# Kernel tuning notes

Hardware: AMD Instinct MI355X
Metric: run time of the kernel (lower is better)

## Reference

```python
import jax, jax.numpy as jnp
import numpy as np

EPSILON = 1e-8
MATCH_THRESHOLD = 0.5
MEANINGFUL_RADIUS = 0.05


def setup_inputs() -> dict:
    key = jax.random.key(0)
    ks = jax.random.split(key, 8)
    B, T, H, D, N = 4, 4096, 2048, 256, 8192
    K = H // 4
    s = lambda k, shape, fan_in: jax.random.normal(k, shape, jnp.float32) * (fan_in ** -0.5)
    return {
        "hidden": jax.random.normal(ks[0], (B, T, H), jnp.float32),
        "beliefs": jax.random.normal(ks[1], (N, D), jnp.float32),
        "active_mask": jax.random.bernoulli(ks[2], 0.9, (N,)),
        "W_obs": s(ks[3], (D, H), H),
        "W_g1": s(ks[4], (K, H), H),
        "b_g1": jnp.zeros((K,), jnp.float32),
        "W_g2": s(ks[5], (1, K), K),
        "b_g2": jnp.full((1,), -2.0, jnp.float32),  # nn.init.constant_(bias, -2.0)
        "W_p1": s(ks[6], (K, H), H),
        "b_p1": jnp.zeros((K,), jnp.float32),
        "W_p2": s(ks[7], (1, K), K),
        "b_p2": jnp.zeros((1,), jnp.float32),
    }


def reference(hidden, beliefs, active_mask, W_obs, W_g1, b_g1, W_g2, b_g2, W_p1, b_p1, W_p2, b_p2):
    # --- projections over [B, T, H] ---
    obs = jnp.einsum('bth,dh->btd', hidden, W_obs)                       # [B,T,D]
    g_h = jax.nn.relu(jnp.einsum('bth,kh->btk', hidden, W_g1) + b_g1)
    gate = jax.nn.sigmoid(jnp.einsum('btk,ok->bto', g_h, W_g2) + b_g2)   # [B,T,1]
    p_h = jax.nn.relu(jnp.einsum('bth,kh->btk', hidden, W_p1) + b_p1)
    prec = jax.nn.softplus(jnp.einsum('btk,ok->bto', p_h, W_p2) + b_p2)  # [B,T,1]

    obs_mean = obs.mean(axis=0)            # [T,D]
    prec_mean = (gate * prec).mean(axis=0)  # [T,1]

    # F.normalize(x, dim=-1, eps) == x / max(||x||, eps)
    obs_angles = obs_mean / jnp.maximum(
        jnp.linalg.norm(obs_mean, axis=-1, keepdims=True), EPSILON)
    obs_beliefs = obs_angles * prec_mean    # [T,D], radius = gated precision

    # --- match against active belief slots (fully vectorized, no per-token loop) ---
    obs_r = jnp.linalg.norm(obs_beliefs, axis=-1)                       # [T]
    obs_ang = obs_beliefs / jnp.maximum(obs_r, EPSILON)[:, None]
    bel_r = jnp.maximum(jnp.linalg.norm(beliefs, axis=-1), EPSILON)     # [N]
    bel_ang = beliefs / bel_r[:, None]

    sims = obs_ang @ bel_ang.T              # [T,N] cosine similarities
    neg = jnp.finfo(sims.dtype).min
    masked = jnp.where(active_mask[None, :], sims, neg)
    any_active = jnp.any(active_mask)
    best_sims = jnp.where(any_active, masked.max(axis=-1), 0.0)         # [T]
    best_idx = jnp.where(any_active, jnp.argmax(masked, axis=-1), -1)   # [T]

    meaningful = obs_r > MEANINGFUL_RADIUS
    matched = meaningful & (best_sims > MATCH_THRESHOLD)
    matched_slot = jnp.where(matched, best_idx, -1)                     # -1 == new slot
    match_sim = jnp.where(matched, best_sims, 0.0)

    # vectorized stand-in for list[WriteCandidate]:
    # belief vectors, per-token match similarity, matched slot id, validity mask
    return obs_beliefs, match_sim, matched_slot, meaningful
```

## Files before the change

### kernel.cpp

```cpp
#include <hip/hip_runtime.h>

constexpr int B = 4, T = 4096, H = 2048, D = 256, KK = 512, N = 8192;
constexpr int BT = B * T;
constexpr int NALL = 1280;
constexpr int CAP = 1024;
constexpr int MCAP = 256;

typedef short bf16x8 __attribute__((ext_vector_type(8)));
typedef float f32x4  __attribute__((ext_vector_type(4)));

__device__ __forceinline__ unsigned short f2bf(float f) {
    unsigned u = __float_as_uint(f);
    return (unsigned short)((u + 0x7fffu + ((u >> 16) & 1u)) >> 16);
}
__device__ __forceinline__ float bf2f(unsigned short h) {
    return __uint_as_float((unsigned)h << 16);
}
__device__ __forceinline__ void async16(const void* g, void* l) {
    __builtin_amdgcn_global_load_lds(
        (const __attribute__((address_space(1))) unsigned int*)g,
        (__attribute__((address_space(3))) unsigned int*)l, 16, 0, 0);
}
__device__ __forceinline__ unsigned long long enc_sim(float s, int idx) {
    unsigned bits = __float_as_uint(s);
    unsigned e32 = (bits & 0x80000000u) ? ~bits : (bits | 0x80000000u);
    return ((unsigned long long)e32 << 32) | (unsigned)(~(unsigned)idx);
}
__device__ __forceinline__ unsigned enc_f32(float s) {
    unsigned b = __float_as_uint(s);
    return (b & 0x80000000u) ? ~b : (b | 0x80000000u);
}
__device__ __forceinline__ float dec_f32(unsigned e) {
    return __uint_as_float((e & 0x80000000u) ? (e & 0x7FFFFFFFu) : ~e);
}

constexpr size_t WS_HB   = 0;
constexpr size_t WS_WB   = WS_HB   + (size_t)BT * H * 2;
constexpr size_t WS_BELB = WS_WB   + (size_t)NALL * H * 2;
constexpr size_t WS_OAB  = WS_BELB + (size_t)N * D * 2;
constexpr size_t WS_OBS  = WS_OAB  + (size_t)T * D * 2;
constexpr size_t WS_B1C  = WS_OBS  + (size_t)T * D * 4;
constexpr size_t WS_W2C  = WS_B1C  + 4096;
constexpr size_t WS_FAC  = WS_W2C  + 4096;
constexpr size_t WS_OBSR = WS_FAC  + 16384;
constexpr size_t WS_FLAG = WS_OBSR + 16384;
constexpr size_t WS_ACTV = WS_FLAG + (size_t)CAP * 4;
constexpr size_t WS_META = WS_ACTV + (size_t)N * 4;
constexpr size_t WS_YG   = WS_META + 256;
constexpr size_t WS_YP   = WS_YG   + (size_t)BT * 4;
constexpr size_t WS_ENC  = WS_YP   + (size_t)BT * 4;
constexpr size_t WS_CNT  = WS_ENC  + (size_t)T * 4;
constexpr size_t WS_MCNT = WS_CNT  + 256;
constexpr size_t WS_MLST = WS_MCNT + 256;
constexpr size_t WS_ZEND = WS_MLST + (size_t)MCAP * 4;
constexpr size_t WS_NEEDF = WS_ZEND;
constexpr size_t WS_ZEROSZ = WS_ZEND - WS_YG;

constexpr int    WTC    = 1280;
constexpr size_t F_WT   = 0;
constexpr size_t F_BEL  = F_WT   + (size_t)H * WTC * 4;
constexpr size_t F_OBS  = F_BEL  + (size_t)N * D * 4;
constexpr size_t F_YG   = F_OBS  + (size_t)T * D * 4;
constexpr size_t F_YP   = F_YG   + (size_t)BT * 4;
constexpr size_t F_OBSR = F_YP   + (size_t)BT * 4;
constexpr size_t F_ENC  = F_OBSR + (size_t)T * 4;
constexpr size_t F_ACT  = F_ENC  + (size_t)T * 8;
constexpr size_t F_META = F_ACT  + (size_t)N * 4;
constexpr size_t F_NEED = F_META + 256;

__global__ void mask_kernel(const unsigned char* raw, int* active, int* meta) {
    __shared__ int s_f32bad, s_nz_nonaligned;
    if (threadIdx.x == 0) { s_f32bad = 0; s_nz_nonaligned = 0; }
    __syncthreads();
    const float* rf = (const float*)raw;
    const int*   ri = (const int*)raw;
    for (int i = threadIdx.x; i < N; i += blockDim.x) {
        unsigned char b = raw[i];
        if ((i & 3) && b) atomicOr(&s_nz_nonaligned, 1);
    }
    for (int e = threadIdx.x; e < N / 4; e += blockDim.x) {
        float f = rf[e]; if (!(f == 0.0f || f == 1.0f)) atomicOr(&s_f32bad, 1);
    }
    __syncthreads();
    int layout;
    if (!s_f32bad)            layout = 2;
    else if (s_nz_nonaligned) layout = 1;
    else                      layout = 0;
    for (int n = threadIdx.x; n < N; n += blockDim.x) {
        int a;
        if (layout == 2)      a = (rf[n] != 0.0f);
        else if (layout == 1) a = (raw[n] != 0);
        else                  a = (ri[n] != 0);
        active[n] = a;
    }
    if (threadIdx.x == 0) meta[0] = layout;
}

__global__ void conv_hidden(const float* hidden, unsigned short* hb) {
    int e = blockIdx.x * 256 + threadIdx.x;
    int row = e >> 8, c8 = (e & 255) * 8;
    const float* src = hidden + (size_t)row * H + c8;
    float4 v0 = *(const float4*)src;
    float4 v1 = *(const float4*)(src + 4);
    uint4 o;
    o.x = f2bf(v0.x) | ((unsigned)f2bf(v0.y) << 16);
    o.y = f2bf(v0.z) | ((unsigned)f2bf(v0.w) << 16);
    o.z = f2bf(v1.x) | ((unsigned)f2bf(v1.y) << 16);
    o.w = f2bf(v1.z) | ((unsigned)f2bf(v1.w) << 16);
    *(uint4*)(hb + (size_t)row * H + c8) = o;
}

__global__ void conv_wb(const float* Wg1, const float* Wp1, const float* Wobs,
                        unsigned short* wb) {
    int e = blockIdx.x * 256 + threadIdx.x;
    int row = e >> 8, c8 = (e & 255) * 8;
    const float* src = (row < 512) ? &Wg1[(size_t)row * H]
                     : (row < 1024) ? &Wp1[(size_t)(row - 512) * H]
                                    : &Wobs[(size_t)(row - 1024) * H];
    float4 v0 = *(const float4*)(src + c8);
    float4 v1 = *(const float4*)(src + c8 + 4);
    uint4 o;
    o.x = f2bf(v0.x) | ((unsigned)f2bf(v0.y) << 16);
    o.y = f2bf(v0.z) | ((unsigned)f2bf(v0.w) << 16);
    o.z = f2bf(v1.x) | ((unsigned)f2bf(v1.y) << 16);
    o.w = f2bf(v1.z) | ((unsigned)f2bf(v1.w) << 16);
    *(uint4*)(wb + (size_t)row * H + c8) = o;
}

__global__ void conv_vec(const float* b_g1, const float* b_p1, const float* W_g2,
                         const float* W_p2, float* b1c, float* w2c) {
    int c = threadIdx.x;
    if (c < 512) { b1c[c] = b_g1[c];       w2c[c] = W_g2[c]; }
    else         { b1c[c] = b_p1[c - 512]; w2c[c] = W_p2[c - 512]; }
}

__global__ void belprep_bf(const float* beliefs, unsigned short* belb) {
    int wave = (blockIdx.x * blockDim.x + threadIdx.x) >> 6;
    int lane = threadIdx.x & 63;
    if (wave >= N) return;
    float4 v = ((const float4*)(beliefs + (size_t)wave * D))[lane];
    float ss = v.x * v.x + v.y * v.y + v.z * v.z + v.w * v.w;
    for (int m = 1; m < 64; m <<= 1) ss += __shfl_xor(ss, m, 64);
    float inv = 1.0f / fmaxf(sqrtf(ss), 1e-8f);
    uint2 o;
    o.x = f2bf(v.x * inv) | ((unsigned)f2bf(v.y * inv) << 16);
    o.y = f2bf(v.z * inv) | ((unsigned)f2bf(v.w * inv) << 16);
    *(uint2*)(belb + (size_t)wave * D + lane * 4) = o;
}

__global__ __launch_bounds__(256) void gemm_mlp_mfma(const unsigned short* Ab, const unsigned short* Bb,
                                                     const float* b1c, const float* w2c,
                                                     float* yg, float* yp) {
    __shared__ unsigned short As[128 * 32];
    __shared__ unsigned short Bs[128 * 32];
    __shared__ float b1s[128], w2s[128];
    int tid = threadIdx.x;
    int mb = blockIdx.x, nb = blockIdx.y;
    int m0 = mb * 128, n0 = nb * 128;
    if (tid < 128) { b1s[tid] = b1c[n0 + tid]; w2s[tid] = w2c[n0 + tid]; }
    int wave = tid >> 6, lane = tid & 63;
    int wr = wave >> 1, wc = wave & 1;
    int quad = lane >> 4, mrow = lane & 15;
    f32x4 acc[4][4] = {};
    const unsigned short* gA = Ab + (size_t)(m0 + (tid >> 2)) * H + (tid & 3) * 8;
    const unsigned short* gB = Bb + (size_t)(n0 + (tid >> 2)) * H + (tid & 3) * 8;
    char* lA = (char*)As + wave * 1024;
    char* lB = (char*)Bs + wave * 1024;
    for (int k0 = 0; k0 < H; k0 += 32) {
        async16(gA + k0, lA);
        async16(gA + (size_t)64 * H + k0, lA + 4096);
        async16(gB + k0, lB);
        async16(gB + (size_t)64 * H + k0, lB + 4096);
        __syncthreads();
        bf16x8 a[4], b[4];
        for (int i = 0; i < 4; i++) a[i] = *(const bf16x8*)&As[(wr * 64 + i * 16 + mrow) * 32 + quad * 8];
        for (int j = 0; j < 4; j++) b[j] = *(const bf16x8*)&Bs[(wc * 64 + j * 16 + mrow) * 32 + quad * 8];
        for (int i = 0; i < 4; i++)
            for (int j = 0; j < 4; j++)
                acc[i][j] = __builtin_amdgcn_mfma_f32_16x16x32_bf16(a[i], b[j], acc[i][j], 0, 0, 0);
        __syncthreads();
    }
    float* y = (nb < 4) ? yg : yp;
    for (int i = 0; i < 4; i++) {
        int row_g = m0 + wr * 64 + i * 16 + quad * 4;
        for (int r = 0; r < 4; r++) {
            float s = 0.0f;
            for (int j = 0; j < 4; j++) {
                int cl = wc * 64 + j * 16 + mrow;
                float z = fmaxf(acc[i][j][r] + b1s[cl], 0.0f);
                s += z * w2s[cl];
            }
            s += __shfl_xor(s, 1); s += __shfl_xor(s, 2);
            s += __shfl_xor(s, 4); s += __shfl_xor(s, 8);
            if (mrow == 0) atomicAdd(&y[row_g + r], s);
        }
    }
}

__global__ __launch_bounds__(512) void gemm_obs_sum(const unsigned short* hb, const unsigned short* wb,
                                                    float* obs_buf) {
    __shared__ unsigned short As[128 * 32];
    __shared__ unsigned short Bs[256 * 32];
    int tid = threadIdx.x;
    int t0 = blockIdx.x * 128;
    int wave = tid >> 6, lane = tid & 63;
    int wr = wave >> 2, wc = wave & 3;
    int quad = lane >> 4, mrow = lane & 15;
    f32x4 acc[4][4] = {};
    int arow = tid >> 2, seg8 = (tid & 3) * 8;
    const unsigned short* hA = hb + (size_t)(t0 + arow) * H + seg8;
    const unsigned short* gB = wb + (size_t)(1024 + (tid >> 2)) * H + (tid & 3) * 8;
    char* lB = (char*)Bs + wave * 1024;
    for (int k0 = 0; k0 < H; k0 += 32) {
        async16(gB + k0, lB);
        async16(gB + (size_t)128 * H + k0, lB + 8192);
        {
            uint4 v0 = *(const uint4*)(hA + k0);
            uint4 v1 = *(const uint4*)(hA + (size_t)T * H + k0);
            uint4 v2 = *(const uint4*)(hA + (size_t)2 * T * H + k0);
            uint4 v3 = *(const uint4*)(hA + (size_t)3 * T * H + k0);
            const unsigned* p0 = (const unsigned*)&v0;
            const unsigned* p1 = (const unsigned*)&v1;
            const unsigned* p2 = (const unsigned*)&v2;
            const unsigned* p3 = (const unsigned*)&v3;
            uint4 o; unsigned* po = (unsigned*)&o;
            for (int q = 0; q < 4; q++) {
                float lo = 0.25f * (bf2f((unsigned short)(p0[q] & 0xFFFF)) + bf2f((unsigned short)(p1[q] & 0xFFFF))
                                  + bf2f((unsigned short)(p2[q] & 0xFFFF)) + bf2f((unsigned short)(p3[q] & 0xFFFF)));
                float hi = 0.25f * (bf2f((unsigned short)(p0[q] >> 16)) + bf2f((unsigned short)(p1[q] >> 16))
                                  + bf2f((unsigned short)(p2[q] >> 16)) + bf2f((unsigned short)(p3[q] >> 16)));
                po[q] = f2bf(lo) | ((unsigned)f2bf(hi) << 16);
            }
            *(uint4*)&As[arow * 32 + seg8] = o;
        }
        __syncthreads();
        bf16x8 a[4], b[4];
        for (int i = 0; i < 4; i++) a[i] = *(const bf16x8*)&As[(wr * 64 + i * 16 + mrow) * 32 + quad * 8];
        for (int j = 0; j < 4; j++) b[j] = *(const bf16x8*)&Bs[(wc * 64 + j * 16 + mrow) * 32 + quad * 8];
        for (int i = 0; i < 4; i++)
            for (int j = 0; j < 4; j++)
                acc[i][j] = __builtin_amdgcn_mfma_f32_16x16x32_bf16(a[i], b[j], acc[i][j], 0, 0, 0);
        __syncthreads();
    }
    for (int i = 0; i < 4; i++)
        for (int r = 0; r < 4; r++) {
            int row_g = t0 + wr * 64 + i * 16 + quad * 4 + r;
            for (int j = 0; j < 4; j++) {
                int col = wc * 64 + j * 16 + mrow;
                obs_buf[(size_t)row_g * D + col] = acc[i][j][r];
            }
        }
}

__global__ void finalize_fast(const float* yg, const float* yp, const float* obs_buf,
                              const float* b_g2, const float* b_p2,
                              float* out0, float* out3, float* obs_r_ws, float* fac,
                              unsigned short* oab, int* flaglist, int* flagcnt,
                              float* yg_mut, float* yp_mut) {
    int t = blockIdx.x * 4 + (threadIdx.x >> 6);
    int lane = threadIdx.x & 63;
    if (t >= T) return;
    float bg2 = b_g2[0], bp2 = b_p2[0];
    float pm = 0.0f;
    for (int b = 0; b < B; ++b) {
        float g = yg[b * T + t] + bg2;
        float p = yp[b * T + t] + bp2;
        float gate = 1.0f / (1.0f + expf(-g));
        float prec = (p > 20.0f) ? p : log1pf(expf(p));
        pm += gate * prec;
    }
    pm *= 0.25f;
    float4 v = ((const float4*)(obs_buf + (size_t)t * D))[lane];
    float ss = v.x * v.x + v.y * v.y + v.z * v.z + v.w * v.w;
    for (int m = 1; m < 64; m <<= 1) ss += __shfl_xor(ss, m, 64);
    float norm = sqrtf(ss);
    float na = fmaxf(norm, 1e-8f);
    float f = norm / na;
    float inv = 1.0f / na;
    float ax = v.x * inv, ay = v.y * inv, az = v.z * inv, aw = v.w * inv;
    float4 ob; ob.x = ax * pm; ob.y = ay * pm; ob.z = az * pm; ob.w = aw * pm;
    ((float4*)(out0 + (size_t)t * D))[lane] = ob;
    uint2 oa;
    oa.x = f2bf(ax) | ((unsigned)f2bf(ay) << 16);
    oa.y = f2bf(az) | ((unsigned)f2bf(aw) << 16);
    *(uint2*)(oab + (size_t)t * D + lane * 4) = oa;
    if (lane == 0) {
        float obs_r = pm * f;
        obs_r_ws[t] = obs_r;
        fac[t] = f;
        out3[t] = (obs_r > 0.05f) ? 1.0f : 0.0f;
        if (fabsf(obs_r - 0.05f) < 5.0e-4f) {
            int idx = atomicAdd(flagcnt, 1);
            if (idx < CAP) {
                flaglist[idx] = t;
                for (int b = 0; b < B; ++b) { yg_mut[b * T + t] = 0.0f; yp_mut[b * T + t] = 0.0f; }
            }
        }
    }
}

__global__ __launch_bounds__(256) void refine_mfma(const float* hidden,
        const float* W_g1, const float* W_p1, const float* b1c, const float* w2c,
        const int* flaglist, const int* flagcnt, float* yg, float* yp) {
    int nrows = min(*flagcnt, CAP) * 4;
    int m0 = blockIdx.x * 64;
    if (m0 >= nrows) return;
    int nb = blockIdx.y;
    int n0 = nb * 128;
    __shared__ unsigned short Ahi[64 * 32], Alo[64 * 32];
    __shared__ unsigned short Bhi[128 * 32], Blo[128 * 32];
    __shared__ int rowg_s[64];
    __shared__ float b1s[128], w2s[128];
    int tid = threadIdx.x;
    if (tid < 64) {
        int fr = m0 + tid;
        int rg = -1;
        if (fr < nrows) { int tok = flaglist[fr >> 2]; rg = (fr & 3) * T + tok; }
        rowg_s[tid] = rg;
    } else if (tid >= 128) {
        int c = tid - 128;
        b1s[c] = b1c[n0 + c]; w2s[c] = w2c[n0 + c];
    }
    __syncthreads();
    const float* Wbase = (n0 < 512) ? W_g1 : W_p1;
    int wofs = n0 & 511;
    int arow = tid >> 2, kseg = (tid & 3) * 8;
    int argr = rowg_s[arow]; if (argr < 0) argr = 0;
    const float* aptr = hidden + (size_t)argr * H + kseg;
    const float* bptr0 = Wbase + (size_t)(wofs + arow) * H + kseg;
    const float* bptr1 = Wbase + (size_t)(wofs + arow + 64) * H + kseg;
    int wave = tid >> 6, lane = tid & 63;
    int quad = lane >> 4, mrow = lane & 15;
    f32x4 acc[4][2] = {};
    for (int k0 = 0; k0 < H; k0 += 32) {
        float xs[8];
        {
            float4 v0 = *(const float4*)(aptr + k0);
            float4 v1 = *(const float4*)(aptr + k0 + 4);
            xs[0]=v0.x; xs[1]=v0.y; xs[2]=v0.z; xs[3]=v0.w;
            xs[4]=v1.x; xs[5]=v1.y; xs[6]=v1.z; xs[7]=v1.w;
            unsigned short hi[8], lo[8];
            for (int q = 0; q < 8; q++) {
                hi[q] = f2bf(xs[q]);
                lo[q] = f2bf(xs[q] - bf2f(hi[q]));
            }
            uint4 ph, pl;
            ph.x = hi[0]|((unsigned)hi[1]<<16); ph.y = hi[2]|((unsigned)hi[3]<<16);
            ph.z = hi[4]|((unsigned)hi[5]<<16); ph.w = hi[6]|((unsigned)hi[7]<<16);
            pl.x = lo[0]|((unsigned)lo[1]<<16); pl.y = lo[2]|((unsigned)lo[3]<<16);
            pl.z = lo[4]|((unsigned)lo[5]<<16); pl.w = lo[6]|((unsigned)lo[7]<<16);
            *(uint4*)&Ahi[arow * 32 + kseg] = ph;
            *(uint4*)&Alo[arow * 32 + kseg] = pl;
        }
        for (int half = 0; half < 2; half++) {
            const float* bp = half ? bptr1 : bptr0;
            float4 v0 = *(const float4*)(bp + k0);
            float4 v1 = *(const float4*)(bp + k0 + 4);
            xs[0]=v0.x; xs[1]=v0.y; xs[2]=v0.z; xs[3]=v0.w;
            xs[4]=v1.x; xs[5]=v1.y; xs[6]=v1.z; xs[7]=v1.w;
            unsigned short hi[8], lo[8];
            for (int q = 0; q < 8; q++) {
                hi[q] = f2bf(xs[q]);
                lo[q] = f2bf(xs[q] - bf2f(hi[q]));
            }
            uint4 ph, pl;
            ph.x = hi[0]|((unsigned)hi[1]<<16); ph.y = hi[2]|((unsigned)hi[3]<<16);
            ph.z = hi[4]|((unsigned)hi[5]<<16); ph.w = hi[6]|((unsigned)hi[7]<<16);
            pl.x = lo[0]|((unsigned)lo[1]<<16); pl.y = lo[2]|((unsigned)lo[3]<<16);
            pl.z = lo[4]|((unsigned)lo[5]<<16); pl.w = lo[6]|((unsigned)lo[7]<<16);
            *(uint4*)&Bhi[(arow + half * 64) * 32 + kseg] = ph;
            *(uint4*)&Blo[(arow + half * 64) * 32 + kseg] = pl;
        }
        __syncthreads();
        bf16x8 ah[4], al[4], bh[2], bl[2];
        for (int i = 0; i < 4; i++) {
            ah[i] = *(const bf16x8*)&Ahi[(i * 16 + mrow) * 32 + quad * 8];
            al[i] = *(const bf16x8*)&Alo[(i * 16 + mrow) * 32 + quad * 8];
        }
        for (int j = 0; j < 2; j++) {
            bh[j] = *(const bf16x8*)&Bhi[(wave * 32 + j * 16 + mrow) * 32 + quad * 8];
            bl[j] = *(const bf16x8*)&Blo[(wave * 32 + j * 16 + mrow) * 32 + quad * 8];
        }
        for (int i = 0; i < 4; i++)
            for (int j = 0; j < 2; j++) {
                acc[i][j] = __builtin_amdgcn_mfma_f32_16x16x32_bf16(al[i], bh[j], acc[i][j], 0, 0, 0);
                acc[i][j] = __builtin_amdgcn_mfma_f32_16x16x32_bf16(ah[i], bl[j], acc[i][j], 0, 0, 0);
                acc[i][j] = __builtin_amdgcn_mfma_f32_16x16x32_bf16(ah[i], bh[j], acc[i][j], 0, 0, 0);
            }
        __syncthreads();
    }
    float* y = (nb < 4) ? yg : yp;
    for (int i = 0; i < 4; i++)
        for (int r = 0; r < 4; r++) {
            int row_l = i * 16 + quad * 4 + r;
            float s = 0.0f;
            for (int j = 0; j < 2; j++) {
                int cl = wave * 32 + j * 16 + mrow;
                float z = fmaxf(acc[i][j][r] + b1s[cl], 0.0f);
                s += z * w2s[cl];
            }
            s += __shfl_xor(s, 1); s += __shfl_xor(s, 2);
            s += __shfl_xor(s, 4); s += __shfl_xor(s, 8);
            if (mrow == 0) {
                int rg = rowg_s[row_l];
                if (rg >= 0) atomicAdd(&y[rg], s);
            }
        }
}

__global__ void refine_pm(const float* yg, const float* yp, const float* b_g2, const float* b_p2,
                          const int* flagcnt, const int* flaglist, const float* fac,
                          float* obs_r_ws, float* out3) {
    int nflag = min(*flagcnt, CAP);
    int idx = blockIdx.x * 64 + threadIdx.x;
    if (idx >= nflag) return;
    int t = flaglist[idx];
    float bg2 = b_g2[0], bp2 = b_p2[0];
    float pm = 0.0f;
    for (int b = 0; b < B; ++b) {
        float g = yg[b * T + t] + bg2;
        float p = yp[b * T + t] + bp2;
        float gate = 1.0f / (1.0f + expf(-g));
        float prec = (p > 20.0f) ? p : log1pf(expf(p));
        pm += gate * prec;
    }
    pm *= 0.25f;
    float obs_r = pm * fac[t];
    obs_r_ws[t] = obs_r;
    out3[t] = (obs_r > 0.05f) ? 1.0f : 0.0f;
}

__global__ __launch_bounds__(256) void sims_mfma(const unsigned short* oab, const unsigned short* belb,
                                                 const int* active, unsigned* encg) {
    __shared__ unsigned short As[128 * 32];
    __shared__ unsigned short Bs[128 * 32];
    __shared__ int acts[128];
    __shared__ unsigned lmax32[128];
    int tid = threadIdx.x;
    int mb = blockIdx.x, nb = blockIdx.y;
    int m0 = mb * 128, n0 = nb * 128;
    if (tid < 128) { acts[tid] = active[n0 + tid]; lmax32[tid] = 0u; }
    int wave = tid >> 6, lane = tid & 63;
    int wr = wave >> 1, wc = wave & 1;
    int quad = lane >> 4, mrow = lane & 15;
    f32x4 acc[4][4] = {};
    const unsigned short* gA = oab + (size_t)(m0 + (tid >> 2)) * D + (tid & 3) * 8;
    const unsigned short* gB = belb + (size_t)(n0 + (tid >> 2)) * D + (tid & 3) * 8;
    char* lA = (char*)As + wave * 1024;
    char* lB = (char*)Bs + wave * 1024;
    for (int k0 = 0; k0 < D; k0 += 32) {
        async16(gA + k0, lA);
        async16(gA + (size_t)64 * D + k0, lA + 4096);
        async16(gB + k0, lB);
        async16(gB + (size_t)64 * D + k0, lB + 4096);
        __syncthreads();
        bf16x8 a[4], b[4];
        for (int i = 0; i < 4; i++) a[i] = *(const bf16x8*)&As[(wr * 64 + i * 16 + mrow) * 32 + quad * 8];
        for (int j = 0; j < 4; j++) b[j] = *(const bf16x8*)&Bs[(wc * 64 + j * 16 + mrow) * 32 + quad * 8];
        for (int i = 0; i < 4; i++)
            for (int j = 0; j < 4; j++)
                acc[i][j] = __builtin_amdgcn_mfma_f32_16x16x32_bf16(a[i], b[j], acc[i][j], 0, 0, 0);
        __syncthreads();
    }
    for (int i = 0; i < 4; i++)
        for (int r = 0; r < 4; r++) {
            int row_l = wr * 64 + i * 16 + quad * 4 + r;
            float m = -3.4e38f;
            for (int j = 0; j < 4; j++) {
                int cl = wc * 64 + j * 16 + mrow;
                if (acts[cl]) m = fmaxf(m, acc[i][j][r]);
            }
            m = fmaxf(m, __shfl_xor(m, 1)); m = fmaxf(m, __shfl_xor(m, 2));
            m = fmaxf(m, __shfl_xor(m, 4)); m = fmaxf(m, __shfl_xor(m, 8));
            if (mrow == 0 && m > -3.3e38f) atomicMax(&lmax32[row_l], enc_f32(m));
        }
    __syncthreads();
    if (tid < 128 && lmax32[tid]) atomicMax(&encg[m0 + tid], lmax32[tid]);
}

__global__ void outw_kernel(const unsigned* encg, const float* obs_r_ws,
                            float* out1, float* out2, int* mcnt, int* mlist) {
    int t = blockIdx.x * 256 + threadIdx.x;
    if (t >= T) return;
    unsigned ev = encg[t];
    float best = (ev == 0u) ? -3.4e38f : dec_f32(ev);
    bool meaningful = obs_r_ws[t] > 0.05f;
    bool matched = meaningful && (best > 0.5f);
    out1[t] = matched ? best : 0.0f;
    out2[t] = -1.0f;
    if (matched) {
        int slot = atomicAdd(mcnt, 1);
        if (slot < MCAP) mlist[slot] = t;
    }
}

__global__ void argmax_kernel(const unsigned short* oab, const unsigned short* belb,
                              const int* active, const int* mcnt, const int* mlist,
                              float* out1, float* out2) {
    int nm = min(*mcnt, MCAP);
    int j = blockIdx.x;
    if (j >= nm) return;
    int t = mlist[j];
    __shared__ float q[256];
    __shared__ unsigned long long red[256];
    if (threadIdx.x < 128) {
        unsigned v = ((const unsigned*)(oab + (size_t)t * D))[threadIdx.x];
        q[threadIdx.x * 2]     = bf2f((unsigned short)(v & 0xFFFF));
        q[threadIdx.x * 2 + 1] = bf2f((unsigned short)(v >> 16));
    }
    __syncthreads();
    float best = -3.4e38f; int bi = -1;
    for (int k = 0; k < N / 256; k++) {
        int n = threadIdx.x + k * 256;
        if (!active[n]) continue;
        const uint4* br = (const uint4*)(belb + (size_t)n * D);
        float s = 0.0f;
        for (int c = 0; c < 32; c++) {
            uint4 v = br[c];
            const unsigned* pv = (const unsigned*)&v;
            for (int w = 0; w < 4; w++) {
                s += q[c * 8 + w * 2]     * bf2f((unsigned short)(pv[w] & 0xFFFF));
                s += q[c * 8 + w * 2 + 1] * bf2f((unsigned short)(pv[w] >> 16));
            }
        }
        if (s > best) { best = s; bi = n; }
    }
    red[threadIdx.x] = (bi >= 0) ? enc_sim(best, bi) : 0ULL;
    __syncthreads();
    for (int st = 128; st > 0; st >>= 1) {
        if (threadIdx.x < st) red[threadIdx.x] = max(red[threadIdx.x], red[threadIdx.x + st]);
        __syncthreads();
    }
    if (threadIdx.x == 0) {
        unsigned long long ev = red[0];
        if (ev) {
            unsigned e32 = (unsigned)(ev >> 32);
            out1[t] = __uint_as_float((e32 & 0x80000000u) ? (e32 & 0x7FFFFFFFu) : ~e32);
            out2[t] = (float)(int)~((unsigned)(ev & 0xFFFFFFFFu));
        }
    }
}

__global__ void f_mask_kernel(const unsigned char* raw, int* active, int* meta) {
    __shared__ int s_f32bad, s_nz_nonaligned;
    if (threadIdx.x == 0) { s_f32bad = 0; s_nz_nonaligned = 0; }
    __syncthreads();
    const float* rf = (const float*)raw;
    const int*   ri = (const int*)raw;
    for (int i = threadIdx.x; i < N; i += blockDim.x) {
        unsigned char b = raw[i];
        if ((i & 3) && b) atomicOr(&s_nz_nonaligned, 1);
    }
    for (int e = threadIdx.x; e < N / 4; e += blockDim.x) {
        float f = rf[e]; if (!(f == 0.0f || f == 1.0f)) atomicOr(&s_f32bad, 1);
    }
    __syncthreads();
    int layout = (!s_f32bad) ? 2 : (s_nz_nonaligned ? 1 : 0);
    for (int n = threadIdx.x; n < N; n += blockDim.x) {
        int a;
        if (layout == 2)      a = (rf[n] != 0.0f);
        else if (layout == 1) a = (raw[n] != 0);
        else                  a = (ri[n] != 0);
        active[n] = a;
    }
    if (threadIdx.x == 0) meta[0] = layout;
}

__global__ void wt_kernel(const float* Wg1, const float* Wp1, const float* Wobs, float* WT) {
    __shared__ float tile[32][33];
    int hb = blockIdx.x * 32, cb = blockIdx.y * 32;
    int x = threadIdx.x & 31, y = threadIdx.x >> 5;
    for (int i = 0; i < 32; i += 8) {
        int c = cb + y + i;
        const float* src = (c < 512) ? &Wg1[(size_t)c * H]
                         : (c < 1024) ? &Wp1[(size_t)(c - 512) * H]
                                      : &Wobs[(size_t)(c - 1024) * H];
        tile[y + i][x] = src[hb + x];
    }
    __syncthreads();
    for (int i = 0; i < 32; i += 8)
        WT[(size_t)(hb + y + i) * WTC + cb + x] = tile[x][y + i];
}

__global__ void belprep_kernel(const float* beliefs, float* bel_ang) {
    int wave = (blockIdx.x * blockDim.x + threadIdx.x) >> 6;
    int lane = threadIdx.x & 63;
    if (wave >= N) return;
    float4 v = ((const float4*)(beliefs + (size_t)wave * D))[lane];
    float ss = v.x * v.x + v.y * v.y + v.z * v.z + v.w * v.w;
    for (int m = 1; m < 64; m <<= 1) ss += __shfl_xor(ss, m, 64);
    float inv = 1.0f / fmaxf(sqrtf(ss), 1e-8f);
    float4 o; o.x = v.x * inv; o.y = v.y * inv; o.z = v.z * inv; o.w = v.w * inv;
    ((float4*)(bel_ang + (size_t)wave * D))[lane] = o;
}

__global__ __launch_bounds__(256) void gemm_obs_kernel(const float* hidden, const float* WT,
                                                       float* obs_mean) {
    __shared__ float As[32][33];
    __shared__ float Ws[32][260];
    int t0 = blockIdx.x * 32;
    int tx = threadIdx.x & 63, ty = threadIdx.x >> 6;
    float acc[8][4] = {};
    for (int h0 = 0; h0 < H; h0 += 32) {
        for (int q = 0; q < 4; ++q) {
            int e = threadIdx.x + q * 256;
            int r = e >> 5, kk = e & 31;
            float s = 0.0f;
            for (int b = 0; b < B; ++b) s += hidden[((size_t)b * T + t0 + r) * H + h0 + kk];
            As[kk][r] = s;
        }
        for (int q = 0; q < 8; ++q) {
            int e4 = threadIdx.x + q * 256;
            int kk = e4 >> 6, c4 = (e4 & 63) * 4;
            *(float4*)&Ws[kk][c4] = *(const float4*)&WT[(size_t)(h0 + kk) * WTC + 1024 + c4];
        }
        __syncthreads();
        for (int kk = 0; kk < 32; ++kk) {
            float a[8], w[4];
            for (int i = 0; i < 8; i++) a[i] = As[kk][ty * 8 + i];
            for (int j = 0; j < 4; j++) w[j] = Ws[kk][tx + 64 * j];
            for (int i = 0; i < 8; i++)
                for (int j = 0; j < 4; j++) acc[i][j] += a[i] * w[j];
        }
        __syncthreads();
    }
    for (int i = 0; i < 8; i++)
        for (int j = 0; j < 4; j++)
            obs_mean[(size_t)(t0 + ty * 8 + i) * D + tx + 64 * j] = acc[i][j] * 0.25f;
}

__global__ __launch_bounds__(512, 4) void gemm_mlp_kernel(
        const float* hidden, const float* WT,
        const float* b1g, const float* b1p, const float* w2g, const float* w2p,
        const float* b2g, const float* b2p, float* yg, float* yp) {
    __shared__ float As[16][65];
    __shared__ float Ws[16][516];
    int R = blockIdx.x * 64;
    int path = blockIdx.y;
    int cbase = path * 512;
    int tx = threadIdx.x & 63, ty = threadIdx.x >> 6;
    float acc[8][8] = {};
    for (int h0 = 0; h0 < H; h0 += 16) {
        {   int r = threadIdx.x >> 3, k2 = (threadIdx.x & 7) * 2;
            float2 v = *(const float2*)&hidden[(size_t)(R + r) * H + h0 + k2];
            As[k2][r] = v.x; As[k2 + 1][r] = v.y; }
        for (int q = 0; q < 4; ++q) {
            int e4 = threadIdx.x + q * 512;
            int kk = e4 >> 7, c4 = (e4 & 127) * 4;
            *(float4*)&Ws[kk][c4] = *(const float4*)&WT[(size_t)(h0 + kk) * WTC + cbase + c4];
        }
        __syncthreads();
        for (int kk = 0; kk < 16; ++kk) {
            float a[8], w[8];
            for (int i = 0; i < 8; i++) a[i] = As[kk][ty * 8 + i];
            for (int j = 0; j < 8; j++) w[j] = Ws[kk][tx + 64 * j];
            for (int i = 0; i < 8; i++)
                for (int j = 0; j < 8; j++) acc[i][j] += a[i] * w[j];
        }
        __syncthreads();
    }
    const float* b1 = path ? b1p : b1g;
    const float* w2 = path ? w2p : w2g;
    float b2 = path ? b2p[0] : b2g[0];
    float part[8];
    for (int i = 0; i < 8; i++) {
        float s = 0.0f;
        for (int j = 0; j < 8; j++) {
            int c = tx + 64 * j;
            float z = fmaxf(acc[i][j] + b1[c], 0.0f);
            s += z * w2[c];
        }
        part[i] = s;
    }
    for (int m = 1; m < 64; m <<= 1)
        for (int i = 0; i < 8; i++) part[i] += __shfl_xor(part[i], m, 64);
    if (tx == 0) {
        float* dst = path ? yp : yg;
        for (int i = 0; i < 8; i++) dst[R + ty * 8 + i] = part[i] + b2;
    }
}

__global__ void finalize_kernel(const float* yg, const float* yp, float* obs,
                                float* out0, float* out3, float* obs_r_ws,
                                unsigned long long* enc) {
    int t = blockIdx.x * 4 + (threadIdx.x >> 6);
    int lane = threadIdx.x & 63;
    if (t >= T) return;
    float pm = 0.0f;
    for (int b = 0; b < B; ++b) {
        float g = yg[b * T + t], p = yp[b * T + t];
        float gate = 1.0f / (1.0f + expf(-g));
        float prec = (p > 15.0f) ? p : log1pf(expf(p));
        pm += gate * prec;
    }
    pm *= (1.0f / B);
    float4 v = ((const float4*)(obs + (size_t)t * D))[lane];
    float ss = v.x * v.x + v.y * v.y + v.z * v.z + v.w * v.w;
    for (int m = 1; m < 64; m <<= 1) ss += __shfl_xor(ss, m, 64);
    float norm = sqrtf(ss);
    float na = fmaxf(norm, 1e-8f);
    float4 ob;
    ob.x = v.x / na * pm; ob.y = v.y / na * pm;
    ob.z = v.z / na * pm; ob.w = v.w / na * pm;
    float obs_r = pm * (norm / na);
    ((float4*)(out0 + (size_t)t * D))[lane] = ob;
    float ra = fmaxf(obs_r, 1e-8f);
    float4 oa;
    oa.x = ob.x / ra; oa.y = ob.y / ra; oa.z = ob.z / ra; oa.w = ob.w / ra;
    ((float4*)(obs + (size_t)t * D))[lane] = oa;
    if (lane == 0) {
        out3[t] = (obs_r > 0.05f) ? 1.0f : 0.0f;
        obs_r_ws[t] = obs_r;
        enc[t] = 0ULL;
    }
}

__global__ __launch_bounds__(256) void sims_kernel(const float* obs_ang, const float* bel_ang,
                                                   const int* active, unsigned long long* enc) {
    __shared__ float Aos[64][68];
    __shared__ float Bbs[64][68];
    __shared__ unsigned long long lmax[64];
    __shared__ int act[64];
    int tb = blockIdx.x * 64, nb = blockIdx.y * 64;
    int tx = threadIdx.x & 15, ty = threadIdx.x >> 4;
    if (threadIdx.x < 64) { lmax[threadIdx.x] = 0ULL; act[threadIdx.x] = active[nb + threadIdx.x]; }
    float acc[4][4] = {};
    for (int d0 = 0; d0 < D; d0 += 64) {
        for (int q = 0; q < 4; ++q) {
            int e4 = threadIdx.x + q * 256;
            int r = e4 >> 4, c4 = (e4 & 15) * 4;
            *(float4*)&Aos[r][c4] = *(const float4*)&obs_ang[(size_t)(tb + r) * D + d0 + c4];
            *(float4*)&Bbs[r][c4] = *(const float4*)&bel_ang[(size_t)(nb + r) * D + d0 + c4];
        }
        __syncthreads();
        for (int dd = 0; dd < 64; ++dd) {
            float a[4], w[4];
            for (int i = 0; i < 4; i++) a[i] = Aos[ty + 16 * i][dd];
            for (int j = 0; j < 4; j++) w[j] = Bbs[tx + 16 * j][dd];
            for (int i = 0; i < 4; i++)
                for (int j = 0; j < 4; j++) acc[i][j] += a[i] * w[j];
        }
        __syncthreads();
    }
    for (int i = 0; i < 4; i++) {
        unsigned long long best = 0ULL;
        for (int j = 0; j < 4; j++) {
            int c = tx + 16 * j;
            if (act[c]) {
                unsigned long long ev = enc_sim(acc[i][j], nb + c);
                if (ev > best) best = ev;
            }
        }
        atomicMax(&lmax[ty + 16 * i], best);
    }
    __syncthreads();
    if (threadIdx.x < 64 && lmax[threadIdx.x])
        atomicMax(&enc[tb + threadIdx.x], lmax[threadIdx.x]);
}

__global__ void f_outw_kernel(const unsigned long long* enc, const float* obs_r_ws,
                              float* out1, float* out2) {
    int t = blockIdx.x * 256 + threadIdx.x;
    if (t >= T) return;
    unsigned long long ev = enc[t];
    float best; int idx;
    if (ev == 0ULL) { best = -3.4e38f; idx = -1; }
    else {
        unsigned int e32 = (unsigned int)(ev >> 32);
        unsigned int bits = (e32 & 0x80000000u) ? (e32 & 0x7FFFFFFFu) : ~e32;
        best = __uint_as_float(bits);
        idx = (int)~((unsigned int)(ev & 0xFFFFFFFFu));
    }
    bool meaningful = obs_r_ws[t] > 0.05f;
    bool matched = meaningful && (best > 0.5f);
    out1[t] = matched ? best : 0.0f;
    out2[t] = matched ? (float)idx : -1.0f;
}

extern "C" void kernel_launch(void* const* d_in, const int* in_sizes, int n_in,
                              void* d_out, int out_size, void* d_ws, size_t ws_size,
                              hipStream_t stream) {
    const float* hidden  = (const float*)d_in[0];
    const float* beliefs = (const float*)d_in[1];
    const unsigned char* mask_raw = (const unsigned char*)d_in[2];
    const float* W_obs = (const float*)d_in[3];
    const float* W_g1  = (const float*)d_in[4];
    const float* b_g1  = (const float*)d_in[5];
    const float* W_g2  = (const float*)d_in[6];
    const float* b_g2  = (const float*)d_in[7];
    const float* W_p1  = (const float*)d_in[8];
    const float* b_p1  = (const float*)d_in[9];
    const float* W_p2  = (const float*)d_in[10];
    const float* b_p2  = (const float*)d_in[11];

    float* out0 = (float*)d_out;
    float* out1 = out0 + (size_t)T * D;
    float* out2 = out1 + T;
    float* out3 = out2 + T;
    char* ws = (char*)d_ws;

    if (ws_size >= WS_NEEDF) {
        unsigned short* hb   = (unsigned short*)(ws + WS_HB);
        unsigned short* wb   = (unsigned short*)(ws + WS_WB);
        unsigned short* belb = (unsigned short*)(ws + WS_BELB);
        unsigned short* oab  = (unsigned short*)(ws + WS_OAB);
        float* obs_buf = (float*)(ws + WS_OBS);
        float* b1c     = (float*)(ws + WS_B1C);
        float* w2c     = (float*)(ws + WS_W2C);
        float* fac     = (float*)(ws + WS_FAC);
        float* obs_r   = (float*)(ws + WS_OBSR);
        int*   flaglist= (int*)(ws + WS_FLAG);
        int*   active  = (int*)(ws + WS_ACTV);
        int*   meta    = (int*)(ws + WS_META);
        float* yg      = (float*)(ws + WS_YG);
        float* yp      = (float*)(ws + WS_YP);
        unsigned* encg = (unsigned*)(ws + WS_ENC);
        int*   flagcnt = (int*)(ws + WS_CNT);
        int*   mcnt    = (int*)(ws + WS_MCNT);
        int*   mlist   = (int*)(ws + WS_MLST);

        hipMemsetAsync(ws + WS_YG, 0, WS_ZEROSZ, stream);
        mask_kernel<<<1, 1024, 0, stream>>>(mask_raw, active, meta);
        conv_vec<<<1, 1024, 0, stream>>>(b_g1, b_p1, W_g2, W_p2, b1c, w2c);
        conv_wb<<<NALL, 256, 0, stream>>>(W_g1, W_p1, W_obs, wb);
        conv_hidden<<<BT, 256, 0, stream>>>(hidden, hb);
        belprep_bf<<<N / 4, 256, 0, stream>>>(beliefs, belb);
        gemm_mlp_mfma<<<dim3(BT / 128, 8), 256, 0, stream>>>(hb, wb, b1c, w2c, yg, yp);
        gemm_obs_sum<<<T / 128, 512, 0, stream>>>(hb, wb, obs_buf);
        finalize_fast<<<T / 4, 256, 0, stream>>>(yg, yp, obs_buf, b_g2, b_p2,
                                                 out0, out3, obs_r, fac, oab,
                                                 flaglist, flagcnt, yg, yp);
        refine_mfma<<<dim3(CAP * 4 / 64, 8), 256, 0, stream>>>(hidden, W_g1, W_p1, b1c, w2c,
                                                               flaglist, flagcnt, yg, yp);
        refine_pm<<<CAP / 64, 64, 0, stream>>>(yg, yp, b_g2, b_p2, flagcnt, flaglist,
                                               fac, obs_r, out3);
        sims_mfma<<<dim3(T / 128, N / 128), 256, 0, stream>>>(oab, belb, active, encg);
        outw_kernel<<<(T + 255) / 256, 256, 0, stream>>>(encg, obs_r, out1, out2, mcnt, mlist);
        argmax_kernel<<<MCAP, 256, 0, stream>>>(oab, belb, active, mcnt, mlist, out1, out2);
        return;
    }

    if (ws_size < F_NEED) return;
    float* WT       = (float*)(ws + F_WT);
    float* bel_ang  = (float*)(ws + F_BEL);
    float* obs_buf  = (float*)(ws + F_OBS);
    float* yg       = (float*)(ws + F_YG);
    float* yp       = (float*)(ws + F_YP);
    float* obs_r_ws = (float*)(ws + F_OBSR);
    unsigned long long* enc = (unsigned long long*)(ws + F_ENC);
    int* active     = (int*)(ws + F_ACT);
    int* meta       = (int*)(ws + F_META);

    f_mask_kernel<<<1, 1024, 0, stream>>>(mask_raw, active, meta);
    wt_kernel<<<dim3(H / 32, WTC / 32), 256, 0, stream>>>(W_g1, W_p1, W_obs, WT);
    belprep_kernel<<<N / 4, 256, 0, stream>>>(beliefs, bel_ang);
    gemm_obs_kernel<<<T / 32, 256, 0, stream>>>(hidden, WT, obs_buf);
    gemm_mlp_kernel<<<dim3(BT / 64, 2), 512, 0, stream>>>(
        hidden, WT, b_g1, b_p1, W_g2, W_p2, b_g2, b_p2, yg, yp);
    finalize_kernel<<<T / 4, 256, 0, stream>>>(yg, yp, obs_buf, out0, out3, obs_r_ws, enc);
    sims_kernel<<<dim3(T / 64, N / 64), 256, 0, stream>>>(obs_buf, bel_ang, active, enc);
    f_outw_kernel<<<(T + 255) / 256, 256, 0, stream>>>(enc, obs_r_ws, out1, out2);
}
```

Baseline: 570.8 us.

## Merge obs projection into MLP GEMM and fuse prep/conversion kernels

The separate observation GEMM ran on only 32 blocks with the batch mean folded into the A load. It is now folded into one big GEMM grid as extra column tiles over all B*T rows, and each tile atomically adds 0.25 times its result into obs_buf. The small prep kernels (mask decode, bias copy, belief normalisation) become one launch, and the hidden and weight bf16 conversions become another. The sims kernel drops its shared-memory max staging and issues global atomicMax directly, but only for values above 0.45. The trade is four times the obs GEMM flops plus millions of float atomics, in exchange for fewer launches and better GPU occupancy.

```diff
diff --git a/kernel.cpp b/kernel.cpp
--- a/kernel.cpp
+++ b/kernel.cpp
@@ -38,15 +38,15 @@
 constexpr size_t WS_WB   = WS_HB   + (size_t)BT * H * 2;
 constexpr size_t WS_BELB = WS_WB   + (size_t)NALL * H * 2;
 constexpr size_t WS_OAB  = WS_BELB + (size_t)N * D * 2;
-constexpr size_t WS_OBS  = WS_OAB  + (size_t)T * D * 2;
-constexpr size_t WS_B1C  = WS_OBS  + (size_t)T * D * 4;
+constexpr size_t WS_B1C  = WS_OAB  + (size_t)T * D * 2;
 constexpr size_t WS_W2C  = WS_B1C  + 4096;
 constexpr size_t WS_FAC  = WS_W2C  + 4096;
 constexpr size_t WS_OBSR = WS_FAC  + 16384;
 constexpr size_t WS_FLAG = WS_OBSR + 16384;
 constexpr size_t WS_ACTV = WS_FLAG + (size_t)CAP * 4;
 constexpr size_t WS_META = WS_ACTV + (size_t)N * 4;
-constexpr size_t WS_YG   = WS_META + 256;
+constexpr size_t WS_OBS  = WS_META + 256;
+constexpr size_t WS_YG   = WS_OBS  + (size_t)T * D * 4;
 constexpr size_t WS_YP   = WS_YG   + (size_t)BT * 4;
 constexpr size_t WS_ENC  = WS_YP   + (size_t)BT * 4;
 constexpr size_t WS_CNT  = WS_ENC  + (size_t)T * 4;
@@ -54,7 +54,7 @@
 constexpr size_t WS_MLST = WS_MCNT + 256;
 constexpr size_t WS_ZEND = WS_MLST + (size_t)MCAP * 4;
 constexpr size_t WS_NEEDF = WS_ZEND;
-constexpr size_t WS_ZEROSZ = WS_ZEND - WS_YG;
+constexpr size_t WS_ZEROSZ = WS_ZEND - WS_OBS;
 
 constexpr int    WTC    = 1280;
 constexpr size_t F_WT   = 0;
@@ -68,55 +68,75 @@
 constexpr size_t F_META = F_ACT  + (size_t)N * 4;
 constexpr size_t F_NEED = F_META + 256;
 
-__global__ void mask_kernel(const unsigned char* raw, int* active, int* meta) {
+__global__ void prep_kernel(const float* beliefs, unsigned short* belb,
+                            const unsigned char* mask_raw, int* active, int* meta,
+                            const float* b_g1, const float* b_p1,
+                            const float* W_g2, const float* W_p2,
+                            float* b1c, float* w2c) {
     __shared__ int s_f32bad, s_nz_nonaligned;
-    if (threadIdx.x == 0) { s_f32bad = 0; s_nz_nonaligned = 0; }
-    __syncthreads();
-    const float* rf = (const float*)raw;
-    const int*   ri = (const int*)raw;
-    for (int i = threadIdx.x; i < N; i += blockDim.x) {
-        unsigned char b = raw[i];
-        if ((i & 3) && b) atomicOr(&s_nz_nonaligned, 1);
-    }
-    for (int e = threadIdx.x; e < N / 4; e += blockDim.x) {
-        float f = rf[e]; if (!(f == 0.0f || f == 1.0f)) atomicOr(&s_f32bad, 1);
-    }
-    __syncthreads();
-    int layout;
-    if (!s_f32bad)            layout = 2;
-    else if (s_nz_nonaligned) layout = 1;
-    else                      layout = 0;
-    for (int n = threadIdx.x; n < N; n += blockDim.x) {
-        int a;
-        if (layout == 2)      a = (rf[n] != 0.0f);
-        else if (layout == 1) a = (raw[n] != 0);
-        else                  a = (ri[n] != 0);
-        active[n] = a;
-    }
-    if (threadIdx.x == 0) meta[0] = layout;
-}
-
-__global__ void conv_hidden(const float* hidden, unsigned short* hb) {
-    int e = blockIdx.x * 256 + threadIdx.x;
-    int row = e >> 8, c8 = (e & 255) * 8;
-    const float* src = hidden + (size_t)row * H + c8;
-    float4 v0 = *(const float4*)src;
-    float4 v1 = *(const float4*)(src + 4);
-    uint4 o;
-    o.x = f2bf(v0.x) | ((unsigned)f2bf(v0.y) << 16);
-    o.y = f2bf(v0.z) | ((unsigned)f2bf(v0.w) << 16);
-    o.z = f2bf(v1.x) | ((unsigned)f2bf(v1.y) << 16);
-    o.w = f2bf(v1.z) | ((unsigned)f2bf(v1.w) << 16);
-    *(uint4*)(hb + (size_t)row * H + c8) = o;
-}
-
-__global__ void conv_wb(const float* Wg1, const float* Wp1, const float* Wobs,
-                        unsigned short* wb) {
-    int e = blockIdx.x * 256 + threadIdx.x;
-    int row = e >> 8, c8 = (e & 255) * 8;
-    const float* src = (row < 512) ? &Wg1[(size_t)row * H]
-                     : (row < 1024) ? &Wp1[(size_t)(row - 512) * H]
-                                    : &Wobs[(size_t)(row - 1024) * H];
+    int blk = blockIdx.x;
+    if (blk < N / 4) {
+        int wave = blk * 4 + (threadIdx.x >> 6);
+        int lane = threadIdx.x & 63;
+        float4 v = ((const float4*)(beliefs + (size_t)wave * D))[lane];
+        float ss = v.x * v.x + v.y * v.y + v.z * v.z + v.w * v.w;
+        for (int m = 1; m < 64; m <<= 1) ss += __shfl_xor(ss, m, 64);
+        float inv = 1.0f / fmaxf(sqrtf(ss), 1e-8f);
+        uint2 o;
+        o.x = f2bf(v.x * inv) | ((unsigned)f2bf(v.y * inv) << 16);
+        o.y = f2bf(v.z * inv) | ((unsigned)f2bf(v.w * inv) << 16);
+        *(uint2*)(belb + (size_t)wave * D + lane * 4) = o;
+        return;
+    }
+    if (blk == N / 4) {
+        if (threadIdx.x == 0) { s_f32bad = 0; s_nz_nonaligned = 0; }
+        __syncthreads();
+        const float* rf = (const float*)mask_raw;
+        const int*   ri = (const int*)mask_raw;
+        for (int i = threadIdx.x; i < N; i += blockDim.x) {
+            unsigned char b = mask_raw[i];
+            if ((i & 3) && b) atomicOr(&s_nz_nonaligned, 1);
+        }
+        for (int e = threadIdx.x; e < N / 4; e += blockDim.x) {
+            float f = rf[e]; if (!(f == 0.0f || f == 1.0f)) atomicOr(&s_f32bad, 1);
+        }
+        __syncthreads();
+        int layout;
+        if (!s_f32bad)            layout = 2;
+        else if (s_nz_nonaligned) layout = 1;
+        else                      layout = 0;
+        for (int n = threadIdx.x; n < N; n += blockDim.x) {
+            int a;
+            if (layout == 2)      a = (rf[n] != 0.0f);
+            else if (layout == 1) a = (mask_raw[n] != 0);
+            else                  a = (ri[n] != 0);
+            active[n] = a;
+        }
+        if (threadIdx.x == 0) meta[0] = layout;
+        return;
+    }
+    for (int c = threadIdx.x; c < 1024; c += blockDim.x) {
+        if (c < 512) { b1c[c] = b_g1[c];       w2c[c] = W_g2[c]; }
+        else         { b1c[c] = b_p1[c - 512]; w2c[c] = W_p2[c - 512]; }
+    }
+}
+
+__global__ void conv_all(const float* hidden, const float* Wg1, const float* Wp1,
+                         const float* Wobs, unsigned short* hb, unsigned short* wb) {
+    int blk = blockIdx.x;
+    int c8 = threadIdx.x * 8;
+    const float* src;
+    unsigned short* dst;
+    if (blk < BT) {
+        src = hidden + (size_t)blk * H;
+        dst = hb + (size_t)blk * H;
+    } else {
+        int row = blk - BT;
+        src = (row < 512) ? &Wg1[(size_t)row * H]
+            : (row < 1024) ? &Wp1[(size_t)(row - 512) * H]
+                           : &Wobs[(size_t)(row - 1024) * H];
+        dst = wb + (size_t)row * H;
+    }
     float4 v0 = *(const float4*)(src + c8);
     float4 v1 = *(const float4*)(src + c8 + 4);
     uint4 o;
@@ -124,40 +144,20 @@
     o.y = f2bf(v0.z) | ((unsigned)f2bf(v0.w) << 16);
     o.z = f2bf(v1.x) | ((unsigned)f2bf(v1.y) << 16);
     o.w = f2bf(v1.z) | ((unsigned)f2bf(v1.w) << 16);
-    *(uint4*)(wb + (size_t)row * H + c8) = o;
-}
-
-__global__ void conv_vec(const float* b_g1, const float* b_p1, const float* W_g2,
-                         const float* W_p2, float* b1c, float* w2c) {
-    int c = threadIdx.x;
-    if (c < 512) { b1c[c] = b_g1[c];       w2c[c] = W_g2[c]; }
-    else         { b1c[c] = b_p1[c - 512]; w2c[c] = W_p2[c - 512]; }
-}
-
-__global__ void belprep_bf(const float* beliefs, unsigned short* belb) {
-    int wave = (blockIdx.x * blockDim.x + threadIdx.x) >> 6;
-    int lane = threadIdx.x & 63;
-    if (wave >= N) return;
-    float4 v = ((const float4*)(beliefs + (size_t)wave * D))[lane];
-    float ss = v.x * v.x + v.y * v.y + v.z * v.z + v.w * v.w;
-    for (int m = 1; m < 64; m <<= 1) ss += __shfl_xor(ss, m, 64);
-    float inv = 1.0f / fmaxf(sqrtf(ss), 1e-8f);
-    uint2 o;
-    o.x = f2bf(v.x * inv) | ((unsigned)f2bf(v.y * inv) << 16);
-    o.y = f2bf(v.z * inv) | ((unsigned)f2bf(v.w * inv) << 16);
-    *(uint2*)(belb + (size_t)wave * D + lane * 4) = o;
-}
-
-__global__ __launch_bounds__(256) void gemm_mlp_mfma(const unsigned short* Ab, const unsigned short* Bb,
-                                                     const float* b1c, const float* w2c,
-                                                     float* yg, float* yp) {
+    *(uint4*)(dst + c8) = o;
+}
+
+__global__ __launch_bounds__(256) void big_gemm(const unsigned short* Ab, const unsigned short* Bb,
+                                                const float* b1c, const float* w2c,
+                                                float* yg, float* yp, float* obs_buf) {
     __shared__ unsigned short As[128 * 32];
     __shared__ unsigned short Bs[128 * 32];
     __shared__ float b1s[128], w2s[128];
     int tid = threadIdx.x;
     int mb = blockIdx.x, nb = blockIdx.y;
     int m0 = mb * 128, n0 = nb * 128;
-    if (tid < 128) { b1s[tid] = b1c[n0 + tid]; w2s[tid] = w2c[n0 + tid]; }
+    bool is_mlp = (nb < 8);
+    if (is_mlp && tid < 128) { b1s[tid] = b1c[n0 + tid]; w2s[tid] = w2c[n0 + tid]; }
     int wave = tid >> 6, lane = tid & 63;
     int wr = wave >> 1, wc = wave & 1;
     int quad = lane >> 4, mrow = lane & 15;
@@ -180,76 +180,33 @@
                 acc[i][j] = __builtin_amdgcn_mfma_f32_16x16x32_bf16(a[i], b[j], acc[i][j], 0, 0, 0);
         __syncthreads();
     }
-    float* y = (nb < 4) ? yg : yp;
-    for (int i = 0; i < 4; i++) {
-        int row_g = m0 + wr * 64 + i * 16 + quad * 4;
-        for (int r = 0; r < 4; r++) {
-            float s = 0.0f;
-            for (int j = 0; j < 4; j++) {
-                int cl = wc * 64 + j * 16 + mrow;
-                float z = fmaxf(acc[i][j][r] + b1s[cl], 0.0f);
-                s += z * w2s[cl];
-            }
-            s += __shfl_xor(s, 1); s += __shfl_xor(s, 2);
-            s += __shfl_xor(s, 4); s += __shfl_xor(s, 8);
-            if (mrow == 0) atomicAdd(&y[row_g + r], s);
-        }
-    }
-}
-
-__global__ __launch_bounds__(512) void gemm_obs_sum(const unsigned short* hb, const unsigned short* wb,
-                                                    float* obs_buf) {
-    __shared__ unsigned short As[128 * 32];
-    __shared__ unsigned short Bs[256 * 32];
-    int tid = threadIdx.x;
-    int t0 = blockIdx.x * 128;
-    int wave = tid >> 6, lane = tid & 63;
-    int wr = wave >> 2, wc = wave & 3;
-    int quad = lane >> 4, mrow = lane & 15;
-    f32x4 acc[4][4] = {};
-    int arow = tid >> 2, seg8 = (tid & 3) * 8;
-    const unsigned short* hA = hb + (size_t)(t0 + arow) * H + seg8;
-    const unsigned short* gB = wb + (size_t)(1024 + (tid >> 2)) * H + (tid & 3) * 8;
-    char* lB = (char*)Bs + wave * 1024;
-    for (int k0 = 0; k0 < H; k0 += 32) {
-        async16(gB + k0, lB);
-        async16(gB + (size_t)128 * H + k0, lB + 8192);
-        {
-            uint4 v0 = *(const uint4*)(hA + k0);
-            uint4 v1 = *(const uint4*)(hA + (size_t)T * H + k0);
-            uint4 v2 = *(const uint4*)(hA + (size_t)2 * T * H + k0);
-            uint4 v3 = *(const uint4*)(hA + (size_t)3 * T * H + k0);
-            const unsigned* p0 = (const unsigned*)&v0;
-            const unsigned* p1 = (const unsigned*)&v1;
-            const unsigned* p2 = (const unsigned*)&v2;
-            const unsigned* p3 = (const unsigned*)&v3;
-            uint4 o; unsigned* po = (unsigned*)&o;
-            for (int q = 0; q < 4; q++) {
-                float lo = 0.25f * (bf2f((unsigned short)(p0[q] & 0xFFFF)) + bf2f((unsigned short)(p1[q] & 0xFFFF))
-                                  + bf2f((unsigned short)(p2[q] & 0xFFFF)) + bf2f((unsigned short)(p3[q] & 0xFFFF)));
-                float hi = 0.25f * (bf2f((unsigned short)(p0[q] >> 16)) + bf2f((unsigned short)(p1[q] >> 16))
-                                  + bf2f((unsigned short)(p2[q] >> 16)) + bf2f((unsigned short)(p3[q] >> 16)));
-                po[q] = f2bf(lo) | ((unsigned)f2bf(hi) << 16);
-            }
-            *(uint4*)&As[arow * 32 + seg8] = o;
-        }
-        __syncthreads();
-        bf16x8 a[4], b[4];
-        for (int i = 0; i < 4; i++) a[i] = *(const bf16x8*)&As[(wr * 64 + i * 16 + mrow) * 32 + quad * 8];
-        for (int j = 0; j < 4; j++) b[j] = *(const bf16x8*)&Bs[(wc * 64 + j * 16 + mrow) * 32 + quad * 8];
+    if (is_mlp) {
+        float* y = (nb < 4) ? yg : yp;
+        for (int i = 0; i < 4; i++) {
+            int row_g = m0 + wr * 64 + i * 16 + quad * 4;
+            for (int r = 0; r < 4; r++) {
+                float s = 0.0f;
+                for (int j = 0; j < 4; j++) {
+                    int cl = wc * 64 + j * 16 + mrow;
+                    float z = fmaxf(acc[i][j][r] + b1s[cl], 0.0f);
+                    s += z * w2s[cl];
+                }
+                s += __shfl_xor(s, 1); s += __shfl_xor(s, 2);
+                s += __shfl_xor(s, 4); s += __shfl_xor(s, 8);
+                if (mrow == 0) atomicAdd(&y[row_g + r], s);
+            }
+        }
+    } else {
         for (int i = 0; i < 4; i++)
-            for (int j = 0; j < 4; j++)
-                acc[i][j] = __builtin_amdgcn_mfma_f32_16x16x32_bf16(a[i], b[j], acc[i][j], 0, 0, 0);
-        __syncthreads();
-    }
-    for (int i = 0; i < 4; i++)
-        for (int r = 0; r < 4; r++) {
-            int row_g = t0 + wr * 64 + i * 16 + quad * 4 + r;
-            for (int j = 0; j < 4; j++) {
-                int col = wc * 64 + j * 16 + mrow;
-                obs_buf[(size_t)row_g * D + col] = acc[i][j][r];
-            }
-        }
+            for (int r = 0; r < 4; r++) {
+                int row_g = m0 + wr * 64 + i * 16 + quad * 4 + r;
+                int t = row_g & (T - 1);
+                for (int j = 0; j < 4; j++) {
+                    int d = n0 - 1024 + wc * 64 + j * 16 + mrow;
+                    atomicAdd(&obs_buf[(size_t)t * D + d], acc[i][j][r] * 0.25f);
+                }
+            }
+    }
 }
 
 __global__ void finalize_fast(const float* yg, const float* yp, const float* obs_buf,
@@ -435,11 +392,10 @@
     __shared__ unsigned short As[128 * 32];
     __shared__ unsigned short Bs[128 * 32];
     __shared__ int acts[128];
-    __shared__ unsigned lmax32[128];
     int tid = threadIdx.x;
     int mb = blockIdx.x, nb = blockIdx.y;
     int m0 = mb * 128, n0 = nb * 128;
-    if (tid < 128) { acts[tid] = active[n0 + tid]; lmax32[tid] = 0u; }
+    if (tid < 128) acts[tid] = active[n0 + tid];
     int wave = tid >> 6, lane = tid & 63;
     int wr = wave >> 1, wc = wave & 1;
     int quad = lane >> 4, mrow = lane & 15;
@@ -464,7 +420,7 @@
     }
     for (int i = 0; i < 4; i++)
         for (int r = 0; r < 4; r++) {
-            int row_l = wr * 64 + i * 16 + quad * 4 + r;
+            int row_g = m0 + wr * 64 + i * 16 + quad * 4 + r;
             float m = -3.4e38f;
             for (int j = 0; j < 4; j++) {
                 int cl = wc * 64 + j * 16 + mrow;
@@ -472,10 +428,8 @@
             }
             m = fmaxf(m, __shfl_xor(m, 1)); m = fmaxf(m, __shfl_xor(m, 2));
             m = fmaxf(m, __shfl_xor(m, 4)); m = fmaxf(m, __shfl_xor(m, 8));
-            if (mrow == 0 && m > -3.3e38f) atomicMax(&lmax32[row_l], enc_f32(m));
-        }
-    __syncthreads();
-    if (tid < 128 && lmax32[tid]) atomicMax(&encg[m0 + tid], lmax32[tid]);
+            if (mrow == 0 && m > 0.45f) atomicMax(&encg[row_g], enc_f32(m));
+        }
 }
 
 __global__ void outw_kernel(const unsigned* encg, const float* obs_r_ws,
@@ -804,7 +758,6 @@
         unsigned short* wb   = (unsigned short*)(ws + WS_WB);
         unsigned short* belb = (unsigned short*)(ws + WS_BELB);
         unsigned short* oab  = (unsigned short*)(ws + WS_OAB);
-        float* obs_buf = (float*)(ws + WS_OBS);
         float* b1c     = (float*)(ws + WS_B1C);
         float* w2c     = (float*)(ws + WS_W2C);
         float* fac     = (float*)(ws + WS_FAC);
@@ -812,6 +765,7 @@
         int*   flaglist= (int*)(ws + WS_FLAG);
         int*   active  = (int*)(ws + WS_ACTV);
         int*   meta    = (int*)(ws + WS_META);
+        float* obs_buf = (float*)(ws + WS_OBS);
         float* yg      = (float*)(ws + WS_YG);
         float* yp      = (float*)(ws + WS_YP);
         unsigned* encg = (unsigned*)(ws + WS_ENC);
@@ -819,14 +773,11 @@
         int*   mcnt    = (int*)(ws + WS_MCNT);
         int*   mlist   = (int*)(ws + WS_MLST);
 
-        hipMemsetAsync(ws + WS_YG, 0, WS_ZEROSZ, stream);
-        mask_kernel<<<1, 1024, 0, stream>>>(mask_raw, active, meta);
-        conv_vec<<<1, 1024, 0, stream>>>(b_g1, b_p1, W_g2, W_p2, b1c, w2c);
-        conv_wb<<<NALL, 256, 0, stream>>>(W_g1, W_p1, W_obs, wb);
-        conv_hidden<<<BT, 256, 0, stream>>>(hidden, hb);
-        belprep_bf<<<N / 4, 256, 0, stream>>>(beliefs, belb);
-        gemm_mlp_mfma<<<dim3(BT / 128, 8), 256, 0, stream>>>(hb, wb, b1c, w2c, yg, yp);
-        gemm_obs_sum<<<T / 128, 512, 0, stream>>>(hb, wb, obs_buf);
+        hipMemsetAsync(ws + WS_OBS, 0, WS_ZEROSZ, stream);
+        prep_kernel<<<N / 4 + 2, 256, 0, stream>>>(beliefs, belb, mask_raw, active, meta,
+                                                   b_g1, b_p1, W_g2, W_p2, b1c, w2c);
+        conv_all<<<BT + NALL, 256, 0, stream>>>(hidden, W_g1, W_p1, W_obs, hb, wb);
+        big_gemm<<<dim3(BT / 128, NALL / 128), 256, 0, stream>>>(hb, wb, b1c, w2c, yg, yp, obs_buf);
         finalize_fast<<<T / 4, 256, 0, stream>>>(yg, yp, obs_buf, b_g2, b_p2,
                                                  out0, out3, obs_r, fac, oab,
                                                  flaglist, flagcnt, yg, yp);
```

Result: faster. 500.1 us (-12.4%).
